# Kernel tuning notes

Measured on AMD Instinct MI355X. Metric: run time of the kernel, lower is better.

Reference implementation:

```python
import jax, jax.numpy as jnp
import numpy as np

N = 65536      # total nodes
D = 256        # score_dim
E = 128        # embed_dim
H = 8          # num_heads
HID = 256      # MLP hidden width
G = 128        # number of graphs (segments)


def setup_inputs() -> dict:
    key = jax.random.key(0)
    ks = jax.random.split(key, 16)
    w = lambda k, shape, s=0.02: jax.random.normal(k, shape, jnp.float32) * s
    return {
        "score_matrix": jax.random.normal(ks[0], (N, D), jnp.float32),
        "x": jax.random.normal(ks[1], (N, D), jnp.float32),  # unused by forward (as in source)
        "batch": jnp.sort(jax.random.randint(ks[2], (N,), 0, G)),
        "pos": jax.random.normal(ks[3], (1, D), jnp.float32),
        "para": jax.random.normal(ks[4], (1, E), jnp.float32),
        # stacked per-head MLP weights (q, k, v): in_dim->256->embed_dim
        "Wq1": w(ks[5], (H, D, HID)), "bq1": jnp.zeros((H, HID), jnp.float32),
        "Wq2": w(ks[6], (H, HID, E)), "bq2": jnp.zeros((H, E), jnp.float32),
        "Wk1": w(ks[7], (H, D, HID)), "bk1": jnp.zeros((H, HID), jnp.float32),
        "Wk2": w(ks[8], (H, HID, E)), "bk2": jnp.zeros((H, E), jnp.float32),
        "Wv1": w(ks[9], (H, D, HID)), "bv1": jnp.zeros((H, HID), jnp.float32),
        "Wv2": w(ks[10], (H, HID, E)), "bv2": jnp.zeros((H, E), jnp.float32),
        # out MLP: (H*E)->256->E
        "Wo1": w(ks[11], (H * E, HID)), "bo1": jnp.zeros((HID,), jnp.float32),
        "Wo2": w(ks[12], (HID, E)), "bo2": jnp.zeros((E,), jnp.float32),
    }


def _head_mlp(xs, W1, b1, W2, b2):
    # xs: [N, D]; W1: [H, D, HID]; W2: [H, HID, E] -> [N, H, E]
    h = jax.nn.relu(jnp.einsum('nd,hdk->nhk', xs, W1) + b1)
    return jnp.einsum('nhk,hke->nhe', h, W2) + b2


def _segment_softmax(src, idx, num_seg):
    # grouped softmax along axis 0 (matches torch scatter_max/scatter_add version)
    m = jax.ops.segment_max(src, idx, num_segments=num_seg)
    ex = jnp.exp(src - m[idx])
    den = jax.ops.segment_sum(ex, idx, num_segments=num_seg)[idx] + 1e-16
    return ex / den


def reference(score_matrix, x, batch, pos, para,
              Wq1, bq1, Wq2, bq2, Wk1, bk1, Wk2, bk2, Wv1, bv1, Wv2, bv2,
              Wo1, bo1, Wo2, bo2):
    sm = score_matrix + pos                                  # [N, D]
    q = _head_mlp(sm, Wq1, bq1, Wq2, bq2)                    # [N, H, E]
    k = _head_mlp(sm, Wk1, bk1, Wk2, bk2)                    # [N, H, E]
    v = _head_mlp(sm, Wv1, bv1, Wv2, bv2)                    # [N, H, E]
    scores = jnp.einsum('nhe,nge->nhg', q, k) / np.float32(np.sqrt(E))  # [N, H, H]
    aw = _segment_softmax(scores, batch, G)                  # [N, H, H]
    s = jnp.einsum('nhg,nge->nhe', aw, v).reshape(sm.shape[0], H * E)   # [N, H*E]
    out = jax.nn.relu(s @ Wo1 + bo1) @ Wo2 + bo2             # [N, E]
    return out + para
```

## Files before the change

### kernel.cpp

```cpp
#include <hip/hip_runtime.h>

#define N_NODES 65536
#define NSEG    128

using s16x8 = __attribute__((ext_vector_type(8))) short;
using s16x4 = __attribute__((ext_vector_type(4))) short;
using f32x4 = __attribute__((ext_vector_type(4))) float;

__device__ __forceinline__ float bf2f(unsigned short s) {
    union { unsigned u; float f; } x; x.u = ((unsigned)s) << 16; return x.f;
}
__device__ __forceinline__ short f2bf(float f) {
    union { float f; unsigned u; } x; x.f = f;
    unsigned r = x.u + 0x7FFFu + ((x.u >> 16) & 1u);
    return (short)(r >> 16);
}
__device__ __forceinline__ void gload_lds16(const void* g, void* lds) {
    __builtin_amdgcn_global_load_lds((const __attribute__((address_space(1))) void*)g,
                                     (__attribute__((address_space(3))) void*)lds, 16, 0, 0);
}


__global__ void prep_sm_kernel(const float* __restrict__ score, const float* __restrict__ pos,
                               short* __restrict__ sm) {
    int i = blockIdx.x * blockDim.x + threadIdx.x;
    int base = i * 4;
    f32x4 s = __builtin_nontemporal_load((const f32x4*)(score + base));
    f32x4 p = *(const f32x4*)(pos + (base & 255));
    s16x4 o;
#pragma unroll
    for (int j = 0; j < 4; ++j) o[j] = f2bf(s[j] + p[j]);
    *(s16x4*)(sm + base) = o;
}

__global__ void transpose_all_kernel(const float* __restrict__ Wq1, const float* __restrict__ Wk1,
                                     const float* __restrict__ Wv1, const float* __restrict__ Wq2,
                                     const float* __restrict__ Wk2, const float* __restrict__ Wv2,
                                     const float* __restrict__ Wo1, const float* __restrict__ Wo2,
                                     short* __restrict__ W1T, short* __restrict__ W2T,
                                     short* __restrict__ Wo1T, short* __restrict__ Wo2T) {
    int t = blockIdx.x;
    const float* in; short* out; int R, C, tx, ty;
    if (t < 1536) {
        int u = t >> 6, rem = t & 63;
        const float* s = (u < 8) ? Wq1 : (u < 16) ? Wk1 : Wv1;
        in = s + (long)(u & 7) * 65536; out = W1T + (long)u * 65536;
        R = 256; C = 256; tx = rem & 7; ty = rem >> 3;
    } else if (t < 2304) {
        int t2 = t - 1536, u = t2 >> 5, rem = t2 & 31;
        const float* s = (u < 8) ? Wq2 : (u < 16) ? Wk2 : Wv2;
        in = s + (long)(u & 7) * 32768; out = W2T + (long)u * 32768;
        R = 256; C = 128; tx = rem & 3; ty = rem >> 2;
    } else if (t < 2560) {
        int t3 = t - 2304;
        in = Wo1; out = Wo1T; R = 1024; C = 256; tx = t3 & 7; ty = t3 >> 3;
    } else {
        int t4 = t - 2560;
        in = Wo2; out = Wo2T; R = 256; C = 128; tx = t4 & 3; ty = t4 >> 2;
    }
    __shared__ float tbuf[32][33];
    const int c0 = tx * 32, r0 = ty * 32;
    const int lx = threadIdx.x & 31, ly = threadIdx.x >> 5;
#pragma unroll
    for (int i = 0; i < 32; i += 8)
        tbuf[ly + i][lx] = in[(long)(r0 + ly + i) * C + c0 + lx];
    __syncthreads();
#pragma unroll
    for (int i = 0; i < 32; i += 8)
        out[(long)(c0 + ly + i) * R + r0 + lx] = f2bf(tbuf[lx][ly + i]);
}

__global__ void prep_small_kernel(const float* __restrict__ bq1, const float* __restrict__ bk1,
                                  const float* __restrict__ bv1, const float* __restrict__ bq2,
                                  const float* __restrict__ bk2, const float* __restrict__ bv2,
                                  const float* __restrict__ bo2, const float* __restrict__ para,
                                  float* __restrict__ b1cat, float* __restrict__ b2cat,
                                  float* __restrict__ bo2p) {
    int i = blockIdx.x * blockDim.x + threadIdx.x;
    if (i < 6144) {
        int u = i >> 8, j = i & 255;
        const float* s = (u < 8) ? (bq1 + u * 256 + j)
                       : (u < 16) ? (bk1 + (u - 8) * 256 + j)
                                  : (bv1 + (u - 16) * 256 + j);
        b1cat[i] = *s;
    } else if (i < 9216) {
        int ii = i - 6144;
        int u = ii >> 7, j = ii & 127;
        const float* s = (u < 8) ? (bq2 + u * 128 + j)
                       : (u < 16) ? (bk2 + (u - 8) * 128 + j)
                                  : (bv2 + (u - 16) * 128 + j);
        b2cat[ii] = *s;
    } else if (i < 9344) {
        int e = i - 9216;
        bo2p[e] = bo2[e] + para[e];
    }
}


template <bool OUTBF16>
__global__ __launch_bounds__(256, 2)
void fused_mlp(const short* __restrict__ A, int lda,
               const short* __restrict__ B1, long b1_ustride,
               const float* __restrict__ bias1, int bias1_ustride,
               const short* __restrict__ B2, long b2_ustride,
               const float* __restrict__ bias2, int bias2_ustride,
               void* __restrict__ Cv, int ldc, long c_ustride, int K1) {
    const int u = blockIdx.y;
    B1    += (long)u * b1_ustride;
    bias1 += (long)u * bias1_ustride;
    B2    += (long)u * b2_ustride;
    bias2 += (long)u * bias2_ustride;

    __shared__ __align__(16) short lds[24576];
    short* Bs = lds;
    short* As = lds + 8192;
    short* hs = lds + 8192;

    const int tid = threadIdx.x, lane = tid & 63, wave = tid >> 6;
    const int wm = wave >> 1, wn = wave & 1;
    const int brow = blockIdx.x * 128;

    const int lrow = lane >> 3;
    const int schk = ((lane & 7) ^ lrow) * 8;
    const int nkt1 = K1 >> 6;
    const int l15 = lane & 15, lq = lane >> 4;

    f32x4 acc2[4][4];
#pragma unroll
    for (int i = 0; i < 4; ++i)
#pragma unroll
        for (int j = 0; j < 4; ++j) acc2[i][j] = (f32x4){0.f, 0.f, 0.f, 0.f};

    for (int p = 0; p < 2; ++p) {
        f32x4 acc1[4][4];
#pragma unroll
        for (int i = 0; i < 4; ++i)
#pragma unroll
            for (int j = 0; j < 4; ++j) acc1[i][j] = (f32x4){0.f, 0.f, 0.f, 0.f};

        for (int kt = 0; kt < nkt1; ++kt) {
            __syncthreads();
            const int ko = kt * 64;
#pragma unroll
            for (int i = 0; i < 4; ++i) {
                int cch = wave * 4 + i;
                int r = cch * 8 + lrow;
                gload_lds16(A  + (long)(brow + r) * lda + ko + schk, &As[cch * 512]);
                gload_lds16(B1 + (long)(p * 128 + r) * K1 + ko + schk, &Bs[cch * 512]);
            }
            __syncthreads();
#pragma unroll
            for (int kk = 0; kk < 2; ++kk) {
                const int slot = (((kk * 4) + lq) ^ (lane & 7)) * 8;
                s16x8 af[4], bfv[4];
#pragma unroll
                for (int i = 0; i < 4; ++i)
                    af[i] = *(const s16x8*)&As[(wm * 64 + i * 16 + l15) * 64 + slot];
#pragma unroll
                for (int j = 0; j < 4; ++j)
                    bfv[j] = *(const s16x8*)&Bs[(wn * 64 + j * 16 + l15) * 64 + slot];
#pragma unroll
                for (int i = 0; i < 4; ++i)
#pragma unroll
                    for (int j = 0; j < 4; ++j)
                        acc1[i][j] = __builtin_amdgcn_mfma_f32_16x16x32_bf16(bfv[j], af[i], acc1[i][j], 0, 0, 0);
            }
        }

        __syncthreads();

        {
            const int cbq = lq << 2;
#pragma unroll
            for (int j = 0; j < 4; ++j) {
                int cb = wn * 64 + j * 16 + cbq;
                f32x4 bv = *(const f32x4*)(bias1 + p * 128 + cb);
#pragma unroll
                for (int i = 0; i < 4; ++i) {
                    int node = wm * 64 + i * 16 + l15;
                    s16x4 hv;
#pragma unroll
                    for (int r = 0; r < 4; ++r)
                        hv[r] = f2bf(fmaxf(acc1[i][j][r] + bv[r], 0.f));
                    *(s16x4*)&hs[node * 128 + (((cb >> 3) ^ (node & 7)) << 3) + (cb & 7)] = hv;
                }
            }
        }

#pragma unroll
        for (int kt2 = 0; kt2 < 2; ++kt2) {
            __syncthreads();
#pragma unroll
            for (int i = 0; i < 4; ++i) {
                int cch = wave * 4 + i;
                int r = cch * 8 + lrow;
                gload_lds16(B2 + (long)r * 256 + p * 128 + kt2 * 64 + schk, &Bs[cch * 512]);
            }
            __syncthreads();
#pragma unroll
            for (int kk = 0; kk < 2; ++kk) {
                const int slotb = (((kk * 4) + lq) ^ (lane & 7)) * 8;
                s16x8 hf[4], wf[4];
#pragma unroll
                for (int i = 0; i < 4; ++i) {
                    int row = wm * 64 + i * 16 + l15;
                    int c = kt2 * 8 + kk * 4 + lq;
                    hf[i] = *(const s16x8*)&hs[row * 128 + ((c ^ (row & 7)) << 3)];
                }
#pragma unroll
                for (int j = 0; j < 4; ++j)
                    wf[j] = *(const s16x8*)&Bs[(wn * 64 + j * 16 + l15) * 64 + slotb];
#pragma unroll
                for (int i = 0; i < 4; ++i)
#pragma unroll
                    for (int j = 0; j < 4; ++j)
                        acc2[i][j] = __builtin_amdgcn_mfma_f32_16x16x32_bf16(wf[j], hf[i], acc2[i][j], 0, 0, 0);
            }
        }
    }

    const int cbq = lq << 2;
    if (OUTBF16) {
        __syncthreads();
        short* Cs = hs;
#pragma unroll
        for (int j = 0; j < 4; ++j) {
            int cb = wn * 64 + j * 16 + cbq;
            f32x4 bv = *(const f32x4*)(bias2 + cb);
#pragma unroll
            for (int i = 0; i < 4; ++i) {
                int node = wm * 64 + i * 16 + l15;
                s16x4 ov;
#pragma unroll
                for (int r = 0; r < 4; ++r) ov[r] = f2bf(acc2[i][j][r] + bv[r]);
                *(s16x4*)&Cs[node * 128 + (((cb >> 3) ^ (node & 7)) << 3) + (cb & 7)] = ov;
            }
        }
        __syncthreads();
        short* cbase = (short*)Cv + u * c_ustride + (long)brow * ldc;
#pragma unroll
        for (int p8 = 0; p8 < 8; ++p8) {
            int g = tid + p8 * 256;
            int row = g >> 4, ck = g & 15;
            s16x8 val = *(const s16x8*)&Cs[row * 128 + ((ck ^ (row & 7)) * 8)];
            *(s16x8*)(cbase + (long)row * ldc + ck * 8) = val;
        }
    } else {
        float* cbase = (float*)Cv + u * c_ustride;
#pragma unroll
        for (int j = 0; j < 4; ++j) {
            int cb = wn * 64 + j * 16 + cbq;
            f32x4 bv = *(const f32x4*)(bias2 + cb);
#pragma unroll
            for (int i = 0; i < 4; ++i) {
                int node = wm * 64 + i * 16 + l15;
                f32x4 o;
#pragma unroll
                for (int r = 0; r < 4; ++r) o[r] = acc2[i][j][r] + bv[r];
                *(f32x4*)&cbase[(long)(brow + node) * ldc + cb] = o;
            }
        }
    }
}


__global__ void scores_mfma_kernel(const short* __restrict__ qk, float* __restrict__ scores,
                                   int nc) {
    const int lane = threadIdx.x & 63;
    int gw = (blockIdx.x * blockDim.x + threadIdx.x) >> 6;
    int nw = (gridDim.x * blockDim.x) >> 6;
    const int npairs = nc >> 1;
    const int r = lane & 15, ks = lane >> 4;
    for (int p = gw; p < npairs; p += nw) {
        const long n0 = (long)p * 2;
        const short* qp = qk + (n0 + (r >> 3)) * 2048 + (r & 7) * 128 + ks * 8;
        const short* kp = qp + 1024;
        f32x4 acc = (f32x4){0.f, 0.f, 0.f, 0.f};
#pragma unroll
        for (int kt = 0; kt < 4; ++kt) {
            s16x8 a = *(const s16x8*)(qp + kt * 32);
            s16x8 b = *(const s16x8*)(kp + kt * 32);
            acc = __builtin_amdgcn_mfma_f32_16x16x32_bf16(a, b, acc, 0, 0, 0);
        }
        const int c = lane & 15, rr0 = (lane >> 4) * 4;
        if ((rr0 >> 3) == (c >> 3)) {
            float* o = scores + (n0 + (rr0 >> 3)) * 64 + (c & 7);
#pragma unroll
            for (int reg = 0; reg < 4; ++reg)
                o[((rr0 & 7) + reg) * 8] = acc[reg] * 0.08838834764831845f;
        }
    }
}

__global__ void segstats1_kernel(const float* __restrict__ scores, const int* __restrict__ batch,
                                 float* __restrict__ pm, float* __restrict__ ps) {
    const int g = blockIdx.x, sl = blockIdx.y;
    int lo = 0, hi = N_NODES;
    while (lo < hi) { int mid = (lo + hi) >> 1; if (batch[mid] < g) lo = mid + 1; else hi = mid; }
    const int start = lo;
    hi = N_NODES;
    while (lo < hi) { int mid = (lo + hi) >> 1; if (batch[mid] <= g) lo = mid + 1; else hi = mid; }
    const int end = lo;
    const int len = end - start;
    const int s0 = start + (len * sl) / 8;
    const int s1 = start + (len * (sl + 1)) / 8;

    const int e = threadIdx.x & 63, sub = threadIdx.x >> 6;
    __shared__ float red[4][64];
    float m = -1e30f;
    for (int n = s0 + sub; n < s1; n += 4)
        m = fmaxf(m, scores[(long)n * 64 + e]);
    red[sub][e] = m;
    __syncthreads();
    m = fmaxf(fmaxf(red[0][e], red[1][e]), fmaxf(red[2][e], red[3][e]));
    __syncthreads();
    float s = 0.f;
    for (int n = s0 + sub; n < s1; n += 4)
        s += expf(scores[(long)n * 64 + e] - m);
    red[sub][e] = s;
    __syncthreads();
    if (sub == 0) {
        int idx = (g * 8 + sl) * 64 + e;
        pm[idx] = m;
        ps[idx] = red[0][e] + red[1][e] + red[2][e] + red[3][e];
    }
}

__global__ void segstats2_kernel(const float* __restrict__ pm, const float* __restrict__ ps,
                                 float* __restrict__ segm, float* __restrict__ segdinv) {
    const int g = blockIdx.x, e = threadIdx.x;
    float M = -1e30f;
#pragma unroll
    for (int sl = 0; sl < 8; ++sl)
        M = fmaxf(M, pm[(g * 8 + sl) * 64 + e]);
    float den = 1e-16f;
#pragma unroll
    for (int sl = 0; sl < 8; ++sl) {
        int idx = (g * 8 + sl) * 64 + e;
        den += ps[idx] * expf(pm[idx] - M);
    }
    segm[g * 64 + e]    = M;
    segdinv[g * 64 + e] = 1.f / den;
}

__global__ void pv_kernel(const short* __restrict__ v, short* __restrict__ sout,
                          const float* __restrict__ scores, const int* __restrict__ batch,
                          const float* __restrict__ segm, const float* __restrict__ segdinv,
                          int n0) {
    __shared__ float aw[16][64];
    const int t = threadIdx.x;
    const int nodeL0 = blockIdx.x * 16;
    {
        int j0 = t * 4;
        int nl = j0 >> 6, e0 = j0 & 63;
        int n = n0 + nodeL0 + nl;
        int b = batch[n];
        f32x4 sc = *(const f32x4*)(scores + (long)n * 64 + e0);
#pragma unroll
        for (int i = 0; i < 4; ++i)
            aw[nl][e0 + i] = expf(sc[i] - segm[b * 64 + e0 + i]) * segdinv[b * 64 + e0 + i];
    }
    __syncthreads();
    const int nl = t >> 4;
    const int ec = (t & 15) * 8;
    const long nloc = nodeL0 + nl;
    const short* vp = v + nloc * 1024 + ec;
    float acc[8][8];
#pragma unroll
    for (int h = 0; h < 8; ++h)
#pragma unroll
        for (int j = 0; j < 8; ++j) acc[h][j] = 0.f;
#pragma unroll
    for (int g = 0; g < 8; ++g) {
        s16x8 vv = *(const s16x8*)(vp + g * 128);
        float vf[8];
#pragma unroll
        for (int j = 0; j < 8; ++j) vf[j] = bf2f((unsigned short)vv[j]);
#pragma unroll
        for (int h = 0; h < 8; ++h) {
            float wgt = aw[nl][h * 8 + g];
#pragma unroll
            for (int j = 0; j < 8; ++j) acc[h][j] += wgt * vf[j];
        }
    }
#pragma unroll
    for (int h = 0; h < 8; ++h) {
        s16x8 o;
#pragma unroll
        for (int j = 0; j < 8; ++j) o[j] = f2bf(acc[h][j]);
        *(s16x8*)(sout + nloc * 1024 + h * 128 + ec) = o;
    }
}


extern "C" void kernel_launch(void* const* d_in, const int* in_sizes, int n_in,
                              void* d_out, int out_size, void* d_ws, size_t ws_size,
                              hipStream_t stream) {
    const float* score = (const float*)d_in[0];
    const int*   batch = (const int*)d_in[2];
    const float* pos   = (const float*)d_in[3];
    const float* para  = (const float*)d_in[4];
    const float* Wq1 = (const float*)d_in[5];
    const float* bq1 = (const float*)d_in[6];
    const float* Wq2 = (const float*)d_in[7];
    const float* bq2 = (const float*)d_in[8];
    const float* Wk1 = (const float*)d_in[9];
    const float* bk1 = (const float*)d_in[10];
    const float* Wk2 = (const float*)d_in[11];
    const float* bk2 = (const float*)d_in[12];
    const float* Wv1 = (const float*)d_in[13];
    const float* bv1 = (const float*)d_in[14];
    const float* Wv2 = (const float*)d_in[15];
    const float* bv2 = (const float*)d_in[16];
    const float* Wo1 = (const float*)d_in[17];
    const float* bo1 = (const float*)d_in[18];
    const float* Wo2 = (const float*)d_in[19];
    const float* bo2 = (const float*)d_in[20];
    float* out = (float*)d_out;
    (void)in_sizes; (void)n_in; (void)out_size;

    char* w = (char*)d_ws;
    short* sm     = (short*)w; w += (size_t)N_NODES * 256 * 2;
    float* scoresb= (float*)w; w += (size_t)N_NODES * 64 * 4;
    short* W1T    = (short*)w; w += (size_t)24 * 256 * 256 * 2;
    short* W2T    = (short*)w; w += (size_t)24 * 128 * 256 * 2;
    short* Wo1T   = (short*)w; w += (size_t)256 * 1024 * 2;
    short* Wo2T   = (short*)w; w += (size_t)128 * 256 * 2;
    float* b1cat  = (float*)w; w += 6144 * 4;
    float* b2cat  = (float*)w; w += 3072 * 4;
    float* bo2p   = (float*)w; w += 1024;
    float* segm   = (float*)w; w += 8192 * 4;
    float* segdi  = (float*)w; w += 8192 * 4;
    float* pm     = (float*)w; w += 65536 * 4;
    float* ps     = (float*)w; w += 65536 * 4;
    size_t persist = (size_t)(w - (char*)d_ws);
    size_t area = ws_size - persist;

    int NC = 32768;
    while (NC > 1024 && (size_t)NC * 4096 > area) NC >>= 1;
    const int nchunks = N_NODES / NC;
    short* X = (short*)w;

    prep_sm_kernel<<<N_NODES * 256 / 4 / 256, 256, 0, stream>>>(score, pos, sm);
    transpose_all_kernel<<<2592, 256, 0, stream>>>(Wq1, Wk1, Wv1, Wq2, Wk2, Wv2, Wo1, Wo2,
                                                   W1T, W2T, Wo1T, Wo2T);
    prep_small_kernel<<<37, 256, 0, stream>>>(bq1, bk1, bv1, bq2, bk2, bv2, bo2, para,
                                              b1cat, b2cat, bo2p);

    for (int c = 0; c < nchunks; ++c) {
        const int n0 = c * NC;
        fused_mlp<true><<<dim3(NC / 128, 16), 256, 0, stream>>>(
            sm + (size_t)n0 * 256, 256, W1T, 65536, b1cat, 256,
            W2T, 32768, b2cat, 128, X, 2048, 128, 256);
        scores_mfma_kernel<<<NC / 8, 256, 0, stream>>>(X, scoresb + (size_t)n0 * 64, NC);
    }

    segstats1_kernel<<<dim3(NSEG, 8), 256, 0, stream>>>(scoresb, batch, pm, ps);
    segstats2_kernel<<<NSEG, 64, 0, stream>>>(pm, ps, segm, segdi);

    {
        short* v = X;
        short* s = X + (size_t)NC * 1024;
        for (int c = 0; c < nchunks; ++c) {
            const int n0 = c * NC;
            fused_mlp<true><<<dim3(NC / 128, 8), 256, 0, stream>>>(
                sm + (size_t)n0 * 256, 256, W1T + 16 * 65536, 65536, b1cat + 16 * 256, 256,
                W2T + 16 * 32768, 32768, b2cat + 16 * 128, 128, v, 1024, 128, 256);
            pv_kernel<<<NC / 16, 256, 0, stream>>>(v, s, scoresb, batch, segm, segdi, n0);
            fused_mlp<false><<<dim3(NC / 128, 1), 256, 0, stream>>>(
                s, 1024, Wo1T, 0, bo1, 0, Wo2T, 0, bo2p, 0,
                out + (size_t)n0 * 128, 128, 0, 1024);
        }
    }
}
```

Baseline: 654.6 us.

## Prefetch second-layer weights early and batch output MLP over all nodes

Inside fused_mlp, the first W2 k-tile load is issued before the hidden-layer epilogue writes to LDS, and the second tile is issued right after the first tile's MFMAs. This overlaps global-to-LDS weight traffic with compute and removes one barrier per tile. On the host side, when workspace allows, the attention output s is kept for all nodes. V-MLP and pv then run in larger chunks, followed by a single output-MLP launch over the whole graph, which cuts launch count and raises per-launch occupancy. The cost is a larger workspace footprint, and the prefetch relies on the barrier ordering staying correct.

```diff
diff --git a/kernel.cpp b/kernel.cpp
--- a/kernel.cpp
+++ b/kernel.cpp
@@ -169,6 +169,13 @@
 
         __syncthreads();
 
+#pragma unroll
+        for (int i = 0; i < 4; ++i) {
+            int cch = wave * 4 + i;
+            int r = cch * 8 + lrow;
+            gload_lds16(B2 + (long)r * 256 + p * 128 + schk, &Bs[cch * 512]);
+        }
+
         {
             const int cbq = lq << 2;
 #pragma unroll
@@ -189,13 +196,6 @@
 
 #pragma unroll
         for (int kt2 = 0; kt2 < 2; ++kt2) {
-            __syncthreads();
-#pragma unroll
-            for (int i = 0; i < 4; ++i) {
-                int cch = wave * 4 + i;
-                int r = cch * 8 + lrow;
-                gload_lds16(B2 + (long)r * 256 + p * 128 + kt2 * 64 + schk, &Bs[cch * 512]);
-            }
             __syncthreads();
 #pragma unroll
             for (int kk = 0; kk < 2; ++kk) {
@@ -215,6 +215,15 @@
 #pragma unroll
                     for (int j = 0; j < 4; ++j)
                         acc2[i][j] = __builtin_amdgcn_mfma_f32_16x16x32_bf16(wf[j], hf[i], acc2[i][j], 0, 0, 0);
+            }
+            if (kt2 == 0) {
+                __syncthreads();
+#pragma unroll
+                for (int i = 0; i < 4; ++i) {
+                    int cch = wave * 4 + i;
+                    int r = cch * 8 + lrow;
+                    gload_lds16(B2 + (long)r * 256 + p * 128 + 64 + schk, &Bs[cch * 512]);
+                }
             }
         }
     }
@@ -458,16 +467,34 @@
     segstats1_kernel<<<dim3(NSEG, 8), 256, 0, stream>>>(scoresb, batch, pm, ps);
     segstats2_kernel<<<NSEG, 64, 0, stream>>>(pm, ps, segm, segdi);
 
-    {
-        short* v = X;
-        short* s = X + (size_t)NC * 1024;
-        for (int c = 0; c < nchunks; ++c) {
-            const int n0 = c * NC;
-            fused_mlp<true><<<dim3(NC / 128, 8), 256, 0, stream>>>(
+    const size_t sfull_bytes = (size_t)N_NODES * 2048;
+    if (area >= sfull_bytes + (size_t)4096 * 2048) {
+        int NCB = 16384;
+        while ((size_t)NCB * 2048 + sfull_bytes > area) NCB >>= 1;
+        short* sfull = (short*)w;
+        short* v     = sfull + (size_t)N_NODES * 1024;
+        for (int c = 0; c < N_NODES / NCB; ++c) {
+            const int n0 = c * NCB;
+            fused_mlp<true><<<dim3(NCB / 128, 8), 256, 0, stream>>>(
                 sm + (size_t)n0 * 256, 256, W1T + 16 * 65536, 65536, b1cat + 16 * 256, 256,
                 W2T + 16 * 32768, 32768, b2cat + 16 * 128, 128, v, 1024, 128, 256);
-            pv_kernel<<<NC / 16, 256, 0, stream>>>(v, s, scoresb, batch, segm, segdi, n0);
-            fused_mlp<false><<<dim3(NC / 128, 1), 256, 0, stream>>>(
+            pv_kernel<<<NCB / 16, 256, 0, stream>>>(v, sfull + (size_t)n0 * 1024,
+                                                    scoresb, batch, segm, segdi, n0);
+        }
+        fused_mlp<false><<<dim3(N_NODES / 128, 1), 256, 0, stream>>>(
+            sfull, 1024, Wo1T, 0, bo1, 0, Wo2T, 0, bo2p, 0, out, 128, 0, 1024);
+    } else {
+        int NCB = 32768;
+        while (NCB > 1024 && (size_t)NCB * 4096 > area) NCB >>= 1;
+        short* v = (short*)w;
+        short* s = v + (size_t)NCB * 1024;
+        for (int c = 0; c < N_NODES / NCB; ++c) {
+            const int n0 = c * NCB;
+            fused_mlp<true><<<dim3(NCB / 128, 8), 256, 0, stream>>>(
+                sm + (size_t)n0 * 256, 256, W1T + 16 * 65536, 65536, b1cat + 16 * 256, 256,
+                W2T + 16 * 32768, 32768, b2cat + 16 * 128, 128, v, 1024, 128, 256);
+            pv_kernel<<<NCB / 16, 256, 0, stream>>>(v, s, scoresb, batch, segm, segdi, n0);
+            fused_mlp<false><<<dim3(NCB / 128, 1), 256, 0, stream>>>(
                 s, 1024, Wo1T, 0, bo1, 0, Wo2T, 0, bo2p, 0,
                 out + (size_t)n0 * 128, 128, 0, 1024);
         }
```

New measurement: 615.8 us. 1.06x faster.
